# Performance work log

Hardware: AMD Instinct MI355X
Metric: run time of the kernel (lower is better)

The kernel has to match this reference:

```python
import jax, jax.numpy as jnp
import numpy as np

B, T, D = 1, 2048, 4096
N, K, H = 32, 8, 128  # num_heads, num_kv_heads, head_dim
ROPE_BASE = 10000
SCALE_FACTOR = 1.0
EPS = 1e-6
NEG_INF = -1e9


def rms_norm(x):
    var = jnp.mean(jnp.square(x), axis=-1, keepdims=True)
    return x * jax.lax.rsqrt(var + EPS)


def apply_rope(x, positions, base_frequency, scale_factor=1.0):
    # x: [B, L, num_heads, H], positions: [B, L]
    head_dim = x.shape[-1]
    fraction = 2.0 * jnp.arange(head_dim // 2, dtype=jnp.float32) / head_dim
    timescale = base_frequency ** fraction  # [H/2]
    sinusoid = positions[..., None].astype(jnp.float32) / timescale  # [B,L,H/2]
    sinusoid = sinusoid[..., None, :] / scale_factor  # [B,L,1,H/2]
    sin, cos = jnp.sin(sinusoid), jnp.cos(sinusoid)
    x1, x2 = jnp.split(x, 2, axis=-1)
    return jnp.concatenate([x1 * cos - x2 * sin, x2 * cos + x1 * sin], axis=-1)


def setup_inputs() -> dict:
    key = jax.random.key(0)
    ks = jax.random.split(key, 7)
    x = jax.random.normal(ks[0], (B, T, D), dtype=jnp.float32)
    segment_pos = jnp.broadcast_to(jnp.arange(T, dtype=jnp.int32)[None, :], (B, T))
    causal = jnp.tril(jnp.ones((T, T), dtype=bool))
    attn_mask = jnp.where(causal, 0.0, NEG_INF).astype(jnp.float32)[None]  # [B,T,S]
    attn_mask = jnp.broadcast_to(attn_mask, (B, T, T))
    q_w = jax.random.normal(ks[1], (N, D, H), dtype=jnp.float32) * (D ** -0.5)
    kv_w = jax.random.normal(ks[2], (2, K, D, H), dtype=jnp.float32) * (D ** -0.5)
    o_w = jax.random.normal(ks[3], (N, H, D), dtype=jnp.float32) * ((N * H) ** -0.5)
    q_scale = jax.random.normal(ks[4], (H,), dtype=jnp.float32) * 0.02  # RMSNorm scale (zeros-init style)
    k_scale = jax.random.normal(ks[5], (H,), dtype=jnp.float32) * 0.02
    return {"x": x, "segment_pos": segment_pos, "attn_mask": attn_mask,
            "q_w": q_w, "kv_w": kv_w, "o_w": o_w,
            "q_scale": q_scale, "k_scale": k_scale}


def reference(x, segment_pos, attn_mask, q_w, kv_w, o_w, q_scale, k_scale):
    # Projections
    q = jnp.einsum('BTD,NDH->BTNH', x, q_w)          # [B,T,N,H]
    kv = jnp.einsum('BSD,CKDH->CBSKH', x, kv_w)      # [2,B,S,K,H]
    k, v = kv[0], kv[1]
    # QK RMSNorm (with scale, (1+scale) convention) and value RMSNorm (no scale)
    q = rms_norm(q) * (1.0 + q_scale)
    k = rms_norm(k) * (1.0 + k_scale)
    v = rms_norm(v)
    # RoPE (standard path: positions are [B,L])
    q = apply_rope(q, segment_pos, ROPE_BASE, SCALE_FACTOR)
    k = apply_rope(k, segment_pos, ROPE_BASE, SCALE_FACTOR)
    # GQA grouping: [B,T,K,G,H]
    G = N // K
    qg = q.reshape(B, T, K, G, H)
    attn_logits = jnp.einsum('btkgh,bskh->bkgts', qg, k)  # [B,K,G,T,S]
    attn_logits = attn_logits + attn_mask[:, None, None, :, :]
    attn_weights = jax.nn.softmax(attn_logits, axis=-1).astype(v.dtype)
    out = jnp.einsum('bkgts,bskh->btkgh', attn_weights, v)  # [B,T,K,G,H]
    out = out.reshape(B, T, N, H)
    return jnp.einsum('BTNH,NHD->BTD', out, o_w)
```

## Files before the change

kernel.cpp:

```cpp
#include <hip/hip_runtime.h>
#include <stdint.h>


typedef __bf16 bf16x8 __attribute__((ext_vector_type(8)));
typedef float  f32x4  __attribute__((ext_vector_type(4)));

__device__ __forceinline__ uint16_t f2bf(float f) {
    union { float f; uint32_t u; } v; v.f = f;
    uint32_t r = v.u + 0x7fffu + ((v.u >> 16) & 1u);
    return (uint16_t)(r >> 16);
}

__device__ __forceinline__ void gload_lds16(const void* g, void* l) {
    __builtin_amdgcn_global_load_lds(
        (const __attribute__((address_space(1))) uint32_t*)g,
        (__attribute__((address_space(3))) uint32_t*)l, 16, 0, 0);
}

__global__ __launch_bounds__(256) void k_cvt_x(const float* __restrict__ x,
                                               uint16_t* __restrict__ xb) {
    int i = (blockIdx.x * 256 + threadIdx.x) * 8;
    int r = i >> 12, k = i & 4095;
    float4 a = *(const float4*)(x + i);
    float4 b = *(const float4*)(x + i + 4);
    uint16_t tmp[8];
    tmp[0] = f2bf(a.x); tmp[1] = f2bf(a.y); tmp[2] = f2bf(a.z); tmp[3] = f2bf(a.w);
    tmp[4] = f2bf(b.x); tmp[5] = f2bf(b.y); tmp[6] = f2bf(b.z); tmp[7] = f2bf(b.w);
    int dst = r * 4096 + (k & ~63) + (((((k >> 3) & 7) ^ (r & 7))) << 3);
    *(uint4*)(xb + dst) = *(uint4*)tmp;
}

__global__ __launch_bounds__(256) void k_prep_wt(const float* __restrict__ qw,
                                                 const float* __restrict__ kvw,
                                                 uint16_t* __restrict__ Wt) {
    const int hx = blockIdx.x, dx = blockIdx.y, m = blockIdx.z;
    const float* src = (m < 32) ? (qw + (size_t)m * 524288)
                                : (kvw + (size_t)(m - 32) * 524288);
    __shared__ uint16_t tile[64][65];
    const int t = threadIdx.x, d0 = dx * 64, h0 = hx * 64;
#pragma unroll
    for (int i = 0; i < 16; ++i) {
        int idx = i * 256 + t, r = idx >> 6, c = idx & 63;
        tile[r][c] = f2bf(src[(size_t)(d0 + r) * 128 + h0 + c]);
    }
    __syncthreads();
#pragma unroll
    for (int it = 0; it < 2; ++it) {
        int slot = it * 256 + t, hr = slot >> 3, cl = slot & 7;
        int R = m * 128 + h0 + hr;
        uint16_t tmp[8];
#pragma unroll
        for (int e = 0; e < 8; ++e) tmp[e] = tile[cl * 8 + e][hr];
        *(uint4*)&Wt[(size_t)R * 4096 + d0 + ((cl ^ (R & 7)) << 3)] = *(uint4*)tmp;
    }
}

__global__ __launch_bounds__(256) void k_prep_ot(const float* __restrict__ ow,
                                                 uint16_t* __restrict__ Ot) {
    const int dx = blockIdx.x, hx = blockIdx.y, n = blockIdx.z;
    const float* src = ow + (size_t)n * 524288;
    __shared__ uint16_t tile[64][65];
    const int t = threadIdx.x, h0 = hx * 64, d0 = dx * 64;
#pragma unroll
    for (int i = 0; i < 16; ++i) {
        int idx = i * 256 + t, r = idx >> 6, c = idx & 63;
        tile[r][c] = f2bf(src[(size_t)(h0 + r) * 4096 + d0 + c]);
    }
    __syncthreads();
#pragma unroll
    for (int it = 0; it < 2; ++it) {
        int slot = it * 256 + t, dr = slot >> 3, cl = slot & 7;
        int R = d0 + dr;
        uint16_t tmp[8];
#pragma unroll
        for (int e = 0; e < 8; ++e) tmp[e] = tile[cl * 8 + e][dr];
        *(uint4*)&Ot[(size_t)R * 4096 + n * 128 + h0 + ((cl ^ (R & 7)) << 3)] = *(uint4*)tmp;
    }
}

__global__ __launch_bounds__(256) void k_gemm(const uint16_t* __restrict__ A,
                                              const uint16_t* __restrict__ Bt,
                                              float* __restrict__ C,
                                              int M, int N, int Kd) {
    __shared__ uint16_t As[128 * 64];
    __shared__ uint16_t Bs[128 * 64];
    const int t = threadIdx.x;
    const int wave = t >> 6, lane = t & 63, l16 = lane & 15, quad = lane >> 4;
    const int wr = wave >> 1, wc = wave & 1;
    const int bm0 = blockIdx.y * 128, bn0 = blockIdx.x * 128;
    const int sw = l16 & 7;

    f32x4 acc[4][4];
    const f32x4 z4 = {0.f, 0.f, 0.f, 0.f};
#pragma unroll
    for (int i = 0; i < 4; ++i)
#pragma unroll
        for (int j = 0; j < 4; ++j) acc[i][j] = z4;

    const size_t laneOff = (size_t)(lane >> 3) * Kd + (lane & 7) * 8;
    const uint16_t* aBase = A  + (size_t)(bm0 + wave * 32) * Kd + laneOff;
    const uint16_t* bBase = Bt + (size_t)(bn0 + wave * 32) * Kd + laneOff;

    for (int kb = 0; kb < Kd; kb += 64) {
        __syncthreads();
#pragma unroll
        for (int j = 0; j < 4; ++j) {
            gload_lds16(aBase + (size_t)j * 8 * Kd + kb, &As[(wave * 32 + j * 8) * 64]);
            gload_lds16(bBase + (size_t)j * 8 * Kd + kb, &Bs[(wave * 32 + j * 8) * 64]);
        }
        __syncthreads();
#pragma unroll
        for (int kc = 0; kc < 2; ++kc) {
            bf16x8 af[4], bf[4];
#pragma unroll
            for (int i = 0; i < 4; ++i)
                af[i] = *(const bf16x8*)&As[(wr * 64 + i * 16 + l16) * 64 + (((kc * 4 + quad) ^ sw) << 3)];
#pragma unroll
            for (int j = 0; j < 4; ++j)
                bf[j] = *(const bf16x8*)&Bs[(wc * 64 + j * 16 + l16) * 64 + (((kc * 4 + quad) ^ sw) << 3)];
#pragma unroll
            for (int i = 0; i < 4; ++i)
#pragma unroll
                for (int j = 0; j < 4; ++j)
                    acc[i][j] = __builtin_amdgcn_mfma_f32_16x16x32_bf16(af[i], bf[j], acc[i][j], 0, 0, 0);
        }
    }
#pragma unroll
    for (int i = 0; i < 4; ++i)
#pragma unroll
        for (int j = 0; j < 4; ++j) {
            int row = bm0 + wr * 64 + i * 16 + quad * 4;
            int col = bn0 + wc * 64 + j * 16 + l16;
            float* cp = C + (size_t)row * N + col;
            cp[0]             = acc[i][j][0];
            cp[(size_t)N]     = acc[i][j][1];
            cp[2 * (size_t)N] = acc[i][j][2];
            cp[3 * (size_t)N] = acc[i][j][3];
        }
}

__global__ __launch_bounds__(256) void k_normrope(const float* __restrict__ C1,
                                                  const int* __restrict__ pos,
                                                  const float* __restrict__ qs,
                                                  const float* __restrict__ ks,
                                                  uint16_t* __restrict__ Q,
                                                  uint16_t* __restrict__ K,
                                                  uint16_t* __restrict__ Vt) {
    const int wave = threadIdx.x >> 6, lane = threadIdx.x & 63;
    const int vid = blockIdx.x * 4 + wave;
    const int tt = vid / 48, j = vid - tt * 48;
    const float* src = C1 + (size_t)tt * 6144 + j * 128;
    float x1 = src[lane], x2 = src[lane + 64];
    float ss = x1 * x1 + x2 * x2;
#pragma unroll
    for (int m = 1; m < 64; m <<= 1) ss += __shfl_xor(ss, m);
    float r = rsqrtf(ss * (1.0f / 128.0f) + 1e-6f);
    if (j < 40) {
        const float* scale = (j < 32) ? qs : ks;
        float y1 = x1 * r * (1.0f + scale[lane]);
        float y2 = x2 * r * (1.0f + scale[lane + 64]);
        float p = (float)pos[tt];
        float ang = p * exp2f((float)lane * -0.20762050593046014f);
        float sn = sinf(ang), cs = cosf(ang);
        float o1 = y1 * cs - y2 * sn;
        float o2 = y2 * cs + y1 * sn;
        uint16_t* dst = (j < 32) ? (Q + ((size_t)j * 2048 + tt) * 128)
                                 : (K + ((size_t)(j - 32) * 2048 + tt) * 128);
        dst[lane] = f2bf(o1); dst[lane + 64] = f2bf(o2);
    } else {
        int kv = j - 40;
        Vt[(size_t)(kv * 128 + lane) * 2048 + tt]      = f2bf(x1 * r);
        Vt[(size_t)(kv * 128 + lane + 64) * 2048 + tt] = f2bf(x2 * r);
    }
}

__global__ __launch_bounds__(256) void k_attn(const uint16_t* __restrict__ Q,
                                              const uint16_t* __restrict__ K,
                                              const uint16_t* __restrict__ Vt,
                                              uint16_t* __restrict__ att) {
    __shared__ uint16_t sK[128 * 128];
    __shared__ uint16_t sV[128 * 128];
    const int p = blockIdx.x, n = blockIdx.y, kk = n >> 2;
    const int t = threadIdx.x, wave = t >> 6, lane = t & 63;
    const int l16 = lane & 15, quad = lane >> 4;
    const f32x4 z4 = {0.f, 0.f, 0.f, 0.f};

    for (int half = 0; half < 2; ++half) {
        const int qt = half ? (31 - p) : p;
        const int q0 = qt * 64;
        const int nk = (qt >> 1) + 1;

        bf16x8 qf[4];
#pragma unroll
        for (int kc = 0; kc < 4; ++kc)
            qf[kc] = *(const bf16x8*)(Q + (size_t)(n * 2048 + q0 + wave * 16 + l16) * 128 + kc * 32 + quad * 8);

        f32x4 O[8];
#pragma unroll
        for (int h = 0; h < 8; ++h) O[h] = z4;
        float mrow[4], lrow[4];
#pragma unroll
        for (int r = 0; r < 4; ++r) { mrow[r] = -INFINITY; lrow[r] = 0.f; }

        for (int st = 0; st < nk; ++st) {
            const int s0 = st * 128;
            __syncthreads();
#pragma unroll
            for (int it = 0; it < 8; ++it) {
                int rr = it * 16 + (t >> 4);
                int cc = (t & 15) * 8;
                int pc = ((cc >> 3) ^ (rr & 15)) << 3;
                *(uint4*)&sK[rr * 128 + pc] = *(const uint4*)(K  + (size_t)(kk * 2048 + s0 + rr) * 128 + cc);
                *(uint4*)&sV[rr * 128 + pc] = *(const uint4*)(Vt + (size_t)(kk * 128 + rr) * 2048 + s0 + cc);
            }
            __syncthreads();

            f32x4 S[8];
#pragma unroll
            for (int jn = 0; jn < 8; ++jn) S[jn] = z4;
#pragma unroll
            for (int jn = 0; jn < 8; ++jn) {
                int krow = jn * 16 + l16;
#pragma unroll
                for (int kc = 0; kc < 4; ++kc) {
                    bf16x8 b = *(const bf16x8*)&sK[krow * 128 + (((kc * 4 + quad) ^ l16) << 3)];
                    S[jn] = __builtin_amdgcn_mfma_f32_16x16x32_bf16(qf[kc], b, S[jn], 0, 0, 0);
                }
            }
            if (st == nk - 1) {
#pragma unroll
                for (int jn = 0; jn < 8; ++jn) {
                    int sc = s0 + jn * 16 + l16;
#pragma unroll
                    for (int r = 0; r < 4; ++r) {
                        int mr = q0 + wave * 16 + quad * 4 + r;
                        if (sc > mr) S[jn][r] = -INFINITY;
                    }
                }
            }
            float alpha[4];
#pragma unroll
            for (int r = 0; r < 4; ++r) {
                float mx = S[0][r];
#pragma unroll
                for (int jn = 1; jn < 8; ++jn) mx = fmaxf(mx, S[jn][r]);
                mx = fmaxf(mx, __shfl_xor(mx, 1));
                mx = fmaxf(mx, __shfl_xor(mx, 2));
                mx = fmaxf(mx, __shfl_xor(mx, 4));
                mx = fmaxf(mx, __shfl_xor(mx, 8));
                float mnew = fmaxf(mrow[r], mx);
                float a = __expf(mrow[r] - mnew);
                mrow[r] = mnew;
                float sum = 0.f;
#pragma unroll
                for (int jn = 0; jn < 8; ++jn) {
                    float e = __expf(S[jn][r] - mnew);
                    S[jn][r] = e;
                    sum += e;
                }
                sum += __shfl_xor(sum, 1);
                sum += __shfl_xor(sum, 2);
                sum += __shfl_xor(sum, 4);
                sum += __shfl_xor(sum, 8);
                lrow[r] = lrow[r] * a + sum;
                alpha[r] = a;
            }
#pragma unroll
            for (int h = 0; h < 8; ++h)
#pragma unroll
                for (int r = 0; r < 4; ++r) O[h][r] *= alpha[r];

            __syncthreads();
#pragma unroll
            for (int jn = 0; jn < 8; ++jn)
#pragma unroll
                for (int r = 0; r < 4; ++r) {
                    int prow = wave * 16 + quad * 4 + r;
                    int pcol = jn * 16 + l16;
                    sK[prow * 128 + ((pcol & 7) | ((((pcol >> 3) ^ prow) & 15) << 3))]
                        = f2bf(S[jn][r]);
                }
            bf16x8 pf[4];
#pragma unroll
            for (int ksv = 0; ksv < 4; ++ksv)
                pf[ksv] = *(const bf16x8*)&sK[(wave * 16 + l16) * 128 + (((ksv * 4 + quad) ^ l16) << 3)];
#pragma unroll
            for (int hj = 0; hj < 8; ++hj) {
                int vrow = hj * 16 + l16;
#pragma unroll
                for (int ksv = 0; ksv < 4; ++ksv) {
                    bf16x8 b = *(const bf16x8*)&sV[vrow * 128 + (((ksv * 4 + quad) ^ l16) << 3)];
                    O[hj] = __builtin_amdgcn_mfma_f32_16x16x32_bf16(pf[ksv], b, O[hj], 0, 0, 0);
                }
            }
        }

        __syncthreads();
        uint16_t* sO = &sK[wave * 2112];
        float inv[4];
#pragma unroll
        for (int r = 0; r < 4; ++r) inv[r] = 1.0f / lrow[r];
#pragma unroll
        for (int hj = 0; hj < 8; ++hj)
#pragma unroll
            for (int r = 0; r < 4; ++r)
                sO[(quad * 4 + r) * 132 + hj * 16 + l16] = f2bf(O[hj][r] * inv[r]);
#pragma unroll
        for (int it = 0; it < 4; ++it) {
            int slot = it * 64 + lane, rloc = slot >> 4, cl = slot & 15;
            bf16x8 v = *(const bf16x8*)&sO[rloc * 132 + cl * 8];
            int R = q0 + wave * 16 + rloc;
            size_t dst = (size_t)R * 4096 + n * 128 + ((cl & 8) << 3) + (((cl & 7) ^ (R & 7)) << 3);
            *(uint4*)&att[dst] = *(uint4*)&v;
        }
    }
}

extern "C" void kernel_launch(void* const* d_in, const int* in_sizes, int n_in,
                              void* d_out, int out_size, void* d_ws, size_t ws_size,
                              hipStream_t stream) {
    const float* x   = (const float*)d_in[0];
    const int*   sp  = (const int*)d_in[1];
    const float* qw  = (const float*)d_in[3];
    const float* kvw = (const float*)d_in[4];
    const float* ow  = (const float*)d_in[5];
    const float* qsc = (const float*)d_in[6];
    const float* ksc = (const float*)d_in[7];
    float* out = (float*)d_out;

    char* ws = (char*)d_ws;
    uint16_t* xb  = (uint16_t*)(ws);
    uint16_t* Wt  = (uint16_t*)(ws + (size_t)(16u << 20));
    float*    C1  = (float*)   (ws + (size_t)(64u << 20));
    uint16_t* Qb  = (uint16_t*)(ws);
    uint16_t* Kb  = (uint16_t*)(ws + (size_t)(16u << 20));
    uint16_t* Vtb = (uint16_t*)(ws + (size_t)(20u << 20));
    uint16_t* Ot  = (uint16_t*)(ws + (size_t)(24u << 20));
    uint16_t* att = (uint16_t*)(ws + (size_t)(64u << 20));

    k_cvt_x   <<<4096, 256, 0, stream>>>(x, xb);
    k_prep_wt <<<dim3(2, 64, 48), 256, 0, stream>>>(qw, kvw, Wt);
    k_gemm    <<<dim3(48, 16), 256, 0, stream>>>(xb, Wt, C1, 2048, 6144, 4096);
    k_normrope<<<24576, 256, 0, stream>>>(C1, sp, qsc, ksc, Qb, Kb, Vtb);
    k_prep_ot <<<dim3(64, 2, 32), 256, 0, stream>>>(ow, Ot);
    k_attn    <<<dim3(16, 32), 256, 0, stream>>>(Qb, Kb, Vtb, att);
    k_gemm    <<<dim3(32, 16), 256, 0, stream>>>(att, Ot, out, 2048, 4096, 4096);
}
```

Before: 603.6 us.

## Fuse QKV norm/RoPE into GEMM epilogue, split-K output GEMM, async attention loads

The QKV projection GEMM now runs RMSNorm, RoPE and the bf16 conversion in its epilogue and writes pre-swizzled Q/K/V directly. This removes the fp32 C1 round trip and the separate per-row norm kernel. The output projection is split along K into two halves plus a reduce kernel, which doubles the block count for better CU occupancy at the cost of an extra partial buffer pass. Attention K/V tile loads switch to direct global-to-LDS loads, with swizzling moved into the producer layout.

```diff
diff --git a/kernel.cpp b/kernel.cpp
--- a/kernel.cpp
+++ b/kernel.cpp
@@ -78,17 +78,158 @@
     }
 }
 
-__global__ __launch_bounds__(256) void k_gemm(const uint16_t* __restrict__ A,
-                                              const uint16_t* __restrict__ Bt,
-                                              float* __restrict__ C,
-                                              int M, int N, int Kd) {
+__global__ __launch_bounds__(256) void k_gemm_qkv(const uint16_t* __restrict__ A,
+                                                  const uint16_t* __restrict__ Bt,
+                                                  const int* __restrict__ pos,
+                                                  const float* __restrict__ qs,
+                                                  const float* __restrict__ ks,
+                                                  uint16_t* __restrict__ Qg,
+                                                  uint16_t* __restrict__ Kg,
+                                                  uint16_t* __restrict__ Vg) {
+    __shared__ __align__(16) char smem[33792];
+    uint16_t* As  = (uint16_t*)smem;
+    uint16_t* Bs  = (uint16_t*)(smem + 16384);
+    float*    X   = (float*)smem;
+    float*    ssq = (float*)(smem + 32768);
+    const int Kd = 4096;
+    const int t = threadIdx.x;
+    const int wave = t >> 6, lane = t & 63, l16 = lane & 15, quad = lane >> 4;
+    const int wr = wave >> 1, wc = wave & 1;
+    const int n = blockIdx.x, bm0 = blockIdx.y * 128, bn0 = n * 128;
+    const int sw = l16 & 7;
+
+    f32x4 acc[4][4];
+    const f32x4 z4 = {0.f, 0.f, 0.f, 0.f};
+#pragma unroll
+    for (int i = 0; i < 4; ++i)
+#pragma unroll
+        for (int j = 0; j < 4; ++j) acc[i][j] = z4;
+
+    const size_t laneOff = (size_t)(lane >> 3) * Kd + (lane & 7) * 8;
+    const uint16_t* aBase = A  + (size_t)(bm0 + wave * 32) * Kd + laneOff;
+    const uint16_t* bBase = Bt + (size_t)(bn0 + wave * 32) * Kd + laneOff;
+
+    for (int kb = 0; kb < Kd; kb += 64) {
+        __syncthreads();
+#pragma unroll
+        for (int j = 0; j < 4; ++j) {
+            gload_lds16(aBase + (size_t)j * 8 * Kd + kb, &As[(wave * 32 + j * 8) * 64]);
+            gload_lds16(bBase + (size_t)j * 8 * Kd + kb, &Bs[(wave * 32 + j * 8) * 64]);
+        }
+        __syncthreads();
+#pragma unroll
+        for (int kc = 0; kc < 2; ++kc) {
+            bf16x8 af[4], bf[4];
+#pragma unroll
+            for (int i = 0; i < 4; ++i)
+                af[i] = *(const bf16x8*)&As[(wr * 64 + i * 16 + l16) * 64 + (((kc * 4 + quad) ^ sw) << 3)];
+#pragma unroll
+            for (int j = 0; j < 4; ++j)
+                bf[j] = *(const bf16x8*)&Bs[(wc * 64 + j * 16 + l16) * 64 + (((kc * 4 + quad) ^ sw) << 3)];
+#pragma unroll
+            for (int i = 0; i < 4; ++i)
+#pragma unroll
+                for (int j = 0; j < 4; ++j)
+                    acc[i][j] = __builtin_amdgcn_mfma_f32_16x16x32_bf16(af[i], bf[j], acc[i][j], 0, 0, 0);
+        }
+    }
+
+#pragma unroll
+    for (int i = 0; i < 4; ++i)
+#pragma unroll
+        for (int r = 0; r < 4; ++r) {
+            float s = 0.f;
+#pragma unroll
+            for (int j = 0; j < 4; ++j) s += acc[i][j][r] * acc[i][j][r];
+            s += __shfl_xor(s, 1); s += __shfl_xor(s, 2);
+            s += __shfl_xor(s, 4); s += __shfl_xor(s, 8);
+            if (l16 == 0) ssq[(wr * 64 + i * 16 + quad * 4 + r) * 2 + wc] = s;
+        }
+    __syncthreads();
+
+    float s1 = 0.f, s2 = 0.f, invts = 0.f;
+    if (n < 40) {
+        const float* sc = (n < 32) ? qs : ks;
+        s1 = 1.0f + sc[lane];
+        s2 = 1.0f + sc[lane + 64];
+        invts = exp2f((float)lane * -0.20762050593046014f);
+    }
+
+#pragma unroll
+    for (int pass = 0; pass < 2; ++pass) {
+        if (wr == pass) {
+#pragma unroll
+            for (int i = 0; i < 4; ++i)
+#pragma unroll
+                for (int j = 0; j < 4; ++j)
+#pragma unroll
+                    for (int r = 0; r < 4; ++r)
+                        X[(i * 16 + quad * 4 + r) * 128 + wc * 64 + j * 16 + l16] = acc[i][j][r];
+        }
+        __syncthreads();
+        for (int rr = 0; rr < 16; ++rr) {
+            int lrow = wave * 16 + rr;
+            int grow = bm0 + pass * 64 + lrow;
+            float rn = rsqrtf((ssq[(pass * 64 + lrow) * 2] + ssq[(pass * 64 + lrow) * 2 + 1])
+                              * 0.0078125f + 1e-6f);
+            float x1 = X[lrow * 128 + lane];
+            float x2 = X[lrow * 128 + lane + 64];
+            if (n < 40) {
+                float y1 = x1 * rn * s1, y2 = x2 * rn * s2;
+                float ang = (float)pos[grow] * invts;
+                float sn = sinf(ang), cs = cosf(ang);
+                X[lrow * 128 + lane]      = y1 * cs - y2 * sn;
+                X[lrow * 128 + lane + 64] = y2 * cs + y1 * sn;
+            } else {
+                X[lrow * 128 + lane]      = x1 * rn;
+                X[lrow * 128 + lane + 64] = x2 * rn;
+            }
+        }
+        __syncthreads();
+        if (n < 40) {
+#pragma unroll
+            for (int it = 0; it < 4; ++it) {
+                int slot = it * 256 + t, lrow = slot >> 4, c = slot & 15;
+                int tg = bm0 + pass * 64 + lrow;
+                f32x4 a = *(f32x4*)&X[lrow * 128 + c * 8];
+                f32x4 b = *(f32x4*)&X[lrow * 128 + c * 8 + 4];
+                uint16_t tmp[8];
+#pragma unroll
+                for (int e = 0; e < 4; ++e) { tmp[e] = f2bf(a[e]); tmp[4 + e] = f2bf(b[e]); }
+                if (n < 32)
+                    *(uint4*)&Qg[((size_t)n * 2048 + tg) * 128 + c * 8] = *(uint4*)tmp;
+                else
+                    *(uint4*)&Kg[((size_t)(n - 32) * 2048 + tg) * 128 + ((c ^ (tg & 15)) << 3)] = *(uint4*)tmp;
+            }
+        } else {
+#pragma unroll
+            for (int it = 0; it < 4; ++it) {
+                int slot = it * 256 + t, h = slot >> 3, scl = slot & 7;
+                int sc = pass * 8 + scl;
+                uint16_t tmp[8];
+#pragma unroll
+                for (int e = 0; e < 8; ++e) tmp[e] = f2bf(X[(scl * 8 + e) * 128 + h]);
+                *(uint4*)&Vg[((size_t)(n - 40) * 128 + h) * 2048 + bm0 + ((sc ^ (h & 15)) << 3)] = *(uint4*)tmp;
+            }
+        }
+        __syncthreads();
+    }
+}
+
+__global__ __launch_bounds__(256) void k_gemm2(const uint16_t* __restrict__ A,
+                                               const uint16_t* __restrict__ Bt,
+                                               float* __restrict__ C0,
+                                               float* __restrict__ C1p,
+                                               int M, int N, int Kd) {
     __shared__ uint16_t As[128 * 64];
     __shared__ uint16_t Bs[128 * 64];
     const int t = threadIdx.x;
     const int wave = t >> 6, lane = t & 63, l16 = lane & 15, quad = lane >> 4;
     const int wr = wave >> 1, wc = wave & 1;
     const int bm0 = blockIdx.y * 128, bn0 = blockIdx.x * 128;
+    const int kz = blockIdx.z;
     const int sw = l16 & 7;
+    float* C = kz ? C1p : C0;
 
     f32x4 acc[4][4];
     const f32x4 z4 = {0.f, 0.f, 0.f, 0.f};
@@ -101,7 +242,8 @@
     const uint16_t* aBase = A  + (size_t)(bm0 + wave * 32) * Kd + laneOff;
     const uint16_t* bBase = Bt + (size_t)(bn0 + wave * 32) * Kd + laneOff;
 
-    for (int kb = 0; kb < Kd; kb += 64) {
+    const int kbeg = kz * (Kd >> 1), kend = kbeg + (Kd >> 1);
+    for (int kb = kbeg; kb < kend; kb += 64) {
         __syncthreads();
 #pragma unroll
         for (int j = 0; j < 4; ++j) {
@@ -139,39 +281,13 @@
         }
 }
 
-__global__ __launch_bounds__(256) void k_normrope(const float* __restrict__ C1,
-                                                  const int* __restrict__ pos,
-                                                  const float* __restrict__ qs,
-                                                  const float* __restrict__ ks,
-                                                  uint16_t* __restrict__ Q,
-                                                  uint16_t* __restrict__ K,
-                                                  uint16_t* __restrict__ Vt) {
-    const int wave = threadIdx.x >> 6, lane = threadIdx.x & 63;
-    const int vid = blockIdx.x * 4 + wave;
-    const int tt = vid / 48, j = vid - tt * 48;
-    const float* src = C1 + (size_t)tt * 6144 + j * 128;
-    float x1 = src[lane], x2 = src[lane + 64];
-    float ss = x1 * x1 + x2 * x2;
-#pragma unroll
-    for (int m = 1; m < 64; m <<= 1) ss += __shfl_xor(ss, m);
-    float r = rsqrtf(ss * (1.0f / 128.0f) + 1e-6f);
-    if (j < 40) {
-        const float* scale = (j < 32) ? qs : ks;
-        float y1 = x1 * r * (1.0f + scale[lane]);
-        float y2 = x2 * r * (1.0f + scale[lane + 64]);
-        float p = (float)pos[tt];
-        float ang = p * exp2f((float)lane * -0.20762050593046014f);
-        float sn = sinf(ang), cs = cosf(ang);
-        float o1 = y1 * cs - y2 * sn;
-        float o2 = y2 * cs + y1 * sn;
-        uint16_t* dst = (j < 32) ? (Q + ((size_t)j * 2048 + tt) * 128)
-                                 : (K + ((size_t)(j - 32) * 2048 + tt) * 128);
-        dst[lane] = f2bf(o1); dst[lane + 64] = f2bf(o2);
-    } else {
-        int kv = j - 40;
-        Vt[(size_t)(kv * 128 + lane) * 2048 + tt]      = f2bf(x1 * r);
-        Vt[(size_t)(kv * 128 + lane + 64) * 2048 + tt] = f2bf(x2 * r);
-    }
+__global__ __launch_bounds__(256) void k_reduce(float* __restrict__ out,
+                                                const float* __restrict__ p) {
+    int i = (blockIdx.x * 256 + threadIdx.x) * 4;
+    float4 a = *(float4*)(out + i);
+    float4 b = *(const float4*)(p + i);
+    a.x += b.x; a.y += b.y; a.z += b.z; a.w += b.w;
+    *(float4*)(out + i) = a;
 }
 
 __global__ __launch_bounds__(256) void k_attn(const uint16_t* __restrict__ Q,
@@ -185,6 +301,9 @@
     const int l16 = lane & 15, quad = lane >> 4;
     const f32x4 z4 = {0.f, 0.f, 0.f, 0.f};
 
+    const uint16_t* Kbase = K  + ((size_t)kk * 2048 + wave * 32 + (lane >> 4)) * 128 + (lane & 15) * 8;
+    const uint16_t* Vbase = Vt + ((size_t)kk * 128  + wave * 32 + (lane >> 4)) * 2048 + (lane & 15) * 8;
+
     for (int half = 0; half < 2; ++half) {
         const int qt = half ? (31 - p) : p;
         const int q0 = qt * 64;
@@ -206,12 +325,9 @@
             const int s0 = st * 128;
             __syncthreads();
 #pragma unroll
-            for (int it = 0; it < 8; ++it) {
-                int rr = it * 16 + (t >> 4);
-                int cc = (t & 15) * 8;
-                int pc = ((cc >> 3) ^ (rr & 15)) << 3;
-                *(uint4*)&sK[rr * 128 + pc] = *(const uint4*)(K  + (size_t)(kk * 2048 + s0 + rr) * 128 + cc);
-                *(uint4*)&sV[rr * 128 + pc] = *(const uint4*)(Vt + (size_t)(kk * 128 + rr) * 2048 + s0 + cc);
+            for (int j = 0; j < 8; ++j) {
+                gload_lds16(Kbase + (size_t)(s0 + j * 4) * 128, &sK[(wave * 32 + j * 4) * 128]);
+                gload_lds16(Vbase + (size_t)j * 4 * 2048 + s0,  &sV[(wave * 32 + j * 4) * 128]);
             }
             __syncthreads();
 
@@ -329,20 +445,20 @@
     float* out = (float*)d_out;
 
     char* ws = (char*)d_ws;
-    uint16_t* xb  = (uint16_t*)(ws);
-    uint16_t* Wt  = (uint16_t*)(ws + (size_t)(16u << 20));
-    float*    C1  = (float*)   (ws + (size_t)(64u << 20));
-    uint16_t* Qb  = (uint16_t*)(ws);
-    uint16_t* Kb  = (uint16_t*)(ws + (size_t)(16u << 20));
-    uint16_t* Vtb = (uint16_t*)(ws + (size_t)(20u << 20));
-    uint16_t* Ot  = (uint16_t*)(ws + (size_t)(24u << 20));
-    uint16_t* att = (uint16_t*)(ws + (size_t)(64u << 20));
-
-    k_cvt_x   <<<4096, 256, 0, stream>>>(x, xb);
-    k_prep_wt <<<dim3(2, 64, 48), 256, 0, stream>>>(qw, kvw, Wt);
-    k_gemm    <<<dim3(48, 16), 256, 0, stream>>>(xb, Wt, C1, 2048, 6144, 4096);
-    k_normrope<<<24576, 256, 0, stream>>>(C1, sp, qsc, ksc, Qb, Kb, Vtb);
-    k_prep_ot <<<dim3(64, 2, 32), 256, 0, stream>>>(ow, Ot);
-    k_attn    <<<dim3(16, 32), 256, 0, stream>>>(Qb, Kb, Vtb, att);
-    k_gemm    <<<dim3(32, 16), 256, 0, stream>>>(att, Ot, out, 2048, 4096, 4096);
-}
+    uint16_t* xb   = (uint16_t*)(ws);
+    uint16_t* Wt   = (uint16_t*)(ws + (size_t)(16u << 20));
+    uint16_t* Qb   = (uint16_t*)(ws + (size_t)(64u << 20));
+    uint16_t* Kb   = (uint16_t*)(ws + (size_t)(80u << 20));
+    uint16_t* Vtb  = (uint16_t*)(ws + (size_t)(84u << 20));
+    uint16_t* att  = (uint16_t*)(ws);
+    uint16_t* Ot   = (uint16_t*)(ws + (size_t)(16u << 20));
+    float*    part = (float*)   (ws + (size_t)(48u << 20));
+
+    k_cvt_x    <<<4096, 256, 0, stream>>>(x, xb);
+    k_prep_wt  <<<dim3(2, 64, 48), 256, 0, stream>>>(qw, kvw, Wt);
+    k_gemm_qkv <<<dim3(48, 16), 256, 0, stream>>>(xb, Wt, sp, qsc, ksc, Qb, Kb, Vtb);
+    k_prep_ot  <<<dim3(64, 2, 32), 256, 0, stream>>>(ow, Ot);
+    k_attn     <<<dim3(16, 32), 256, 0, stream>>>(Qb, Kb, Vtb, att);
+    k_gemm2    <<<dim3(32, 16, 2), 256, 0, stream>>>(att, Ot, out, part, 2048, 4096, 4096);
+    k_reduce   <<<8192, 256, 0, stream>>>(out, part);
+}
```

New measurement: 586.3 us. 1.03x faster.
